# Optimization experiments

Measured on AMD Instinct MI355X. Metric: run time of the kernel, lower is better.

## Reference

```python
import jax, jax.numpy as jnp
import numpy as np

KERNEL_MUL = 2.0
KERNEL_NUM = 5


def setup_inputs() -> dict:
    key = jax.random.key(0)
    k1, k2 = jax.random.split(key)
    N, D = 4096, 256
    source = jax.random.normal(k1, (N, D), dtype=jnp.float32)
    target = jax.random.normal(k2, (N, D), dtype=jnp.float32)
    return {"source": source, "target": target}


def reference(source, target):
    ns = source.shape[0]
    total = jnp.concatenate([source, target], axis=0)  # [2N, D]
    n = total.shape[0]
    # Pairwise squared L2 distance via GEMM trick (same math as expand+sub+square+sum)
    sq = jnp.sum(total * total, axis=1)               # [2N]
    gram = total @ total.T                             # [2N, 2N]
    l2 = sq[:, None] + sq[None, :] - 2.0 * gram        # [2N, 2N]
    # Bandwidth from detached distances (torch uses .data)
    l2_sg = jax.lax.stop_gradient(l2)
    bandwidth = jnp.sum(l2_sg) / (n * n - n)
    bandwidth = bandwidth / (KERNEL_MUL ** (KERNEL_NUM // 2))
    bws = bandwidth * (KERNEL_MUL ** jnp.arange(KERNEL_NUM, dtype=l2.dtype))  # [K]
    # Multi-kernel Gaussian RBF sum: sum_k exp(-l2 / bw_k)
    kernels = jnp.exp(-l2[None, :, :] / bws[:, None, None]).sum(axis=0)  # [2N, 2N]
    XX = kernels[:ns, :ns]
    YY = kernels[ns:, ns:]
    XY = kernels[:ns, ns:]
    YX = kernels[ns:, :ns]
    loss = jnp.mean(XX) + jnp.mean(YY) - jnp.mean(XY) - jnp.mean(YX)
    return loss
```

## Files before the change

### kernel.cpp

```cpp
#include <hip/hip_runtime.h>
#include <hip/hip_bf16.h>
#include <stdint.h>


#define NROW 8192
#define NS   4096
#define DD   256
#define TILE 256
#define BK   64
#define NTB  32
#define NBLK (NTB*(NTB+1)/2)
#define K1B  128

typedef __bf16 bf16_t;
typedef __bf16 bf16x8 __attribute__((ext_vector_type(8)));
typedef __bf16 bf16x4 __attribute__((ext_vector_type(4)));
typedef float  f32x4  __attribute__((ext_vector_type(4)));
typedef float  f32x2  __attribute__((ext_vector_type(2)));

#define OFF_CPAR 0
#define OFF_SQ   1024
#define OFF_CS   (OFF_SQ + 8192*4)
#define OFF_SS   (OFF_CS + K1B*256*4)
#define OFF_TBF  (1<<18)

__device__ __forceinline__ void async16(const void* g, void* l) {
  __builtin_amdgcn_global_load_lds(
      (const __attribute__((address_space(1))) void*)(uintptr_t)g,
      (__attribute__((address_space(3))) void*)(uintptr_t)l, 16, 0, 0);
}

__global__ __launch_bounds__(256) void k1_prep(const float* __restrict__ src,
                                               const float* __restrict__ tgt,
                                               float* __restrict__ sq,
                                               float* __restrict__ cs_part,
                                               float* __restrict__ ss_part,
                                               bf16_t* __restrict__ tbf,
                                               float* __restrict__ out) {
  const int b = blockIdx.x, tid = threadIdx.x;
  const int w = tid >> 6, lane = tid & 63;
  if (b == 0 && tid == 0) out[0] = 0.f;
  float4 csum = make_float4(0.f, 0.f, 0.f, 0.f);
  float wss = 0.f;
  for (int r = 0; r < 16; ++r) {
    const int row = b * 64 + w * 16 + r;
    const float* rp = (row < NS) ? (src + (size_t)row * DD)
                                 : (tgt + (size_t)(row - NS) * DD);
    float4 v = ((const float4*)rp)[lane];
    bf16x4 o;
    o[0] = (bf16_t)v.x; o[1] = (bf16_t)v.y; o[2] = (bf16_t)v.z; o[3] = (bf16_t)v.w;
    *(bf16x4*)(tbf + (size_t)row * DD + lane * 4) = o;
    float s2 = v.x*v.x + v.y*v.y + v.z*v.z + v.w*v.w;
    #pragma unroll
    for (int off = 32; off >= 1; off >>= 1) s2 += __shfl_xor(s2, off);
    if (lane == 0) { sq[row] = s2; wss += s2; }
    csum.x += v.x; csum.y += v.y; csum.z += v.z; csum.w += v.w;
  }
  __shared__ float cls[4][256];
  __shared__ float sls[4];
  ((float4*)cls[w])[lane] = csum;
  if (lane == 0) sls[w] = wss;
  __syncthreads();
  cs_part[b * 256 + tid] = cls[0][tid] + cls[1][tid] + cls[2][tid] + cls[3][tid];
  if (tid == 0) ss_part[b] = sls[0] + sls[1] + sls[2] + sls[3];
}

__global__ __launch_bounds__(256) void k2_bw(const float* __restrict__ cs_part,
                                             const float* __restrict__ ss_part,
                                             float* __restrict__ cpar) {
  const int tid = threadIdx.x, w = tid >> 6, lane = tid & 63;
  float c = 0.f;
  for (int b = 0; b < K1B; ++b) c += cs_part[b * 256 + tid];
  double csq = (double)c * (double)c;
  double ssq = (tid < K1B) ? (double)ss_part[tid] : 0.0;
  #pragma unroll
  for (int off = 32; off >= 1; off >>= 1) {
    csq += __shfl_xor(csq, off);
    ssq += __shfl_xor(ssq, off);
  }
  __shared__ double rc[4], rs[4];
  if (lane == 0) { rc[w] = csq; rs[w] = ssq; }
  __syncthreads();
  if (tid == 0) {
    double C = rc[0] + rc[1] + rc[2] + rc[3];
    double S = rs[0] + rs[1] + rs[2] + rs[3];
    const double n = (double)NROW;
    double suml2 = 2.0 * n * S - 2.0 * C;
    double bw0 = suml2 / (n * n - n) / 4.0;
    cpar[0] = (float)(1.4426950408889634 / (16.0 * bw0));
  }
}

__global__ __launch_bounds__(512) void k3_mmd(const bf16_t* __restrict__ tbf,
                                              const float* __restrict__ sqg,
                                              const float* __restrict__ cpar,
                                              float* __restrict__ out) {
  __shared__ __align__(16) bf16_t As[TILE * BK];
  __shared__ __align__(16) bf16_t Bs[TILE * BK];
  __shared__ float red[8];

  const int t = blockIdx.x;
  int bi = (int)((sqrtf(8.0f * (float)t + 1.0f) - 1.0f) * 0.5f);
  while ((bi + 1) * (bi + 2) / 2 <= t) ++bi;
  while (bi * (bi + 1) / 2 > t) --bi;
  const int bj = t - bi * (bi + 1) / 2;

  const int tid = threadIdx.x;
  const int w = tid >> 6, lane = tid & 63;
  const int m0 = (w >> 2) * 128;
  const int n0 = (w & 3) * 64;
  const int wbase = tid & ~63;

  const float cE = cpar[0];

  f32x4 acc[8][4] = {};

  const bf16_t* Ag = tbf + (size_t)bi * TILE * DD;
  const bf16_t* Bg = tbf + (size_t)bj * TILE * DD;

  for (int kt = 0; kt < 4; ++kt) {
    __syncthreads();
    #pragma unroll
    for (int it = 0; it < 4; ++it) {
      const int c   = it * 512 + tid;
      const int r   = c >> 3;
      const int kcs = (c & 7) ^ (r & 7);
      async16(Ag + (size_t)r * DD + kt * 64 + kcs * 8,
              (char*)As + (size_t)(it * 512 + wbase) * 16);
      async16(Bg + (size_t)r * DD + kt * 64 + kcs * 8,
              (char*)Bs + (size_t)(it * 512 + wbase) * 16);
    }
    __syncthreads();
    #pragma unroll
    for (int kk = 0; kk < 2; ++kk) {
      const int kc = kk * 4 + (lane >> 4);
      const int kphys = (kc ^ (lane & 7)) * 8;
      bf16x8 af[8], bfr[4];
      #pragma unroll
      for (int mi = 0; mi < 8; ++mi)
        af[mi] = *(const bf16x8*)(As + (m0 + mi * 16 + (lane & 15)) * BK + kphys);
      #pragma unroll
      for (int ni = 0; ni < 4; ++ni)
        bfr[ni] = *(const bf16x8*)(Bs + (n0 + ni * 16 + (lane & 15)) * BK + kphys);
      #pragma unroll
      for (int mi = 0; mi < 8; ++mi)
        #pragma unroll
        for (int ni = 0; ni < 4; ++ni)
          acc[mi][ni] = __builtin_amdgcn_mfma_f32_16x16x32_bf16(
              af[mi], bfr[ni], acc[mi][ni], 0, 0, 0);
    }
  }

  const f32x2 c2 = {2.0f * cE, 2.0f * cE};
  f32x2 bj2[4];
  #pragma unroll
  for (int ni = 0; ni < 4; ++ni) {
    const float b = sqg[bj * TILE + n0 + ni * 16 + (lane & 15)] * cE;
    bj2[ni][0] = b; bj2[ni][1] = b;
  }

  f32x2 t2 = {0.f, 0.f};
  #pragma unroll
  for (int mi = 0; mi < 8; ++mi) {
    const int mbase = bi * TILE + m0 + mi * 16 + (lane >> 4) * 4;
    f32x2 ai2[2];
    ai2[0][0] = sqg[mbase + 0] * cE; ai2[0][1] = sqg[mbase + 1] * cE;
    ai2[1][0] = sqg[mbase + 2] * cE; ai2[1][1] = sqg[mbase + 3] * cE;
    #pragma unroll
    for (int ni = 0; ni < 4; ++ni) {
      #pragma unroll
      for (int h = 0; h < 2; ++h) {
        f32x2 g; g[0] = acc[mi][ni][2*h]; g[1] = acc[mi][ni][2*h+1];
        f32x2 e = g * c2 - (ai2[h] + bj2[ni]);
        f32x2 v;
        v[0] = __builtin_amdgcn_exp2f(e[0]);
        v[1] = __builtin_amdgcn_exp2f(e[1]);
        f32x2 v2 = v * v, v4 = v2 * v2, v8 = v4 * v4, v16 = v8 * v8;
        t2 += ((v + v2) + (v4 + v8)) + v16;
      }
    }
  }
  float tsum = t2[0] + t2[1];
  #pragma unroll
  for (int off = 32; off >= 1; off >>= 1) tsum += __shfl_xor(tsum, off);
  if (lane == 0) red[w] = tsum;
  __syncthreads();
  if (tid == 0) {
    float s = 0.f;
    #pragma unroll
    for (int i = 0; i < 8; ++i) s += red[i];
    const float sign = ((bi < NS / TILE) == (bj < NS / TILE)) ? 1.f : -1.f;
    const float wt   = (bi == bj) ? 1.f : 2.f;
    atomicAdd(out, s * sign * wt * (1.0f / ((float)NS * (float)NS)));
  }
}

extern "C" void kernel_launch(void* const* d_in, const int* in_sizes, int n_in,
                              void* d_out, int out_size, void* d_ws, size_t ws_size,
                              hipStream_t stream) {
  const float* src = (const float*)d_in[0];
  const float* tgt = (const float*)d_in[1];
  char* ws = (char*)d_ws;
  float*  cpar = (float*)(ws + OFF_CPAR);
  float*  sq   = (float*)(ws + OFF_SQ);
  float*  csp  = (float*)(ws + OFF_CS);
  float*  ssp  = (float*)(ws + OFF_SS);
  bf16_t* tbf  = (bf16_t*)(ws + OFF_TBF);
  float*  out  = (float*)d_out;

  k1_prep<<<K1B, 256, 0, stream>>>(src, tgt, sq, csp, ssp, tbf, out);
  k2_bw  <<<1,   256, 0, stream>>>(csp, ssp, cpar);
  k3_mmd <<<NBLK,512, 0, stream>>>(tbf, sq, cpar, out);
}
```

Baseline: 110.4 us.

## Pre-swizzle bf16 operands into MFMA fragment layout and drop LDS staging

The prep kernel now writes the bf16 copy of the inputs in a blocked layout matching the 16x16x32 MFMA operand fragments, so each lane loads its fragment directly from global memory with one 16-byte load. The GEMM kernel drops the LDS tiles, async loads and barriers, and switches to 128x128 tiles with 256 threads, giving about four times as many triangular blocks. The aim is to remove LDS round-trips and synchronisation and to spread work over more blocks, at the cost of more redundant global/L2 traffic, since each fragment is re-read by several waves and blocks without sharing.

```diff
diff --git a/kernel.cpp b/kernel.cpp
--- a/kernel.cpp
+++ b/kernel.cpp
@@ -6,15 +6,12 @@
 #define NROW 8192
 #define NS   4096
 #define DD   256
-#define TILE 256
-#define BK   64
-#define NTB  32
+#define NTB  64
 #define NBLK (NTB*(NTB+1)/2)
 #define K1B  128
 
 typedef __bf16 bf16_t;
 typedef __bf16 bf16x8 __attribute__((ext_vector_type(8)));
-typedef __bf16 bf16x4 __attribute__((ext_vector_type(4)));
 typedef float  f32x4  __attribute__((ext_vector_type(4)));
 typedef float  f32x2  __attribute__((ext_vector_type(2)));
 
@@ -23,12 +20,6 @@
 #define OFF_CS   (OFF_SQ + 8192*4)
 #define OFF_SS   (OFF_CS + K1B*256*4)
 #define OFF_TBF  (1<<18)
-
-__device__ __forceinline__ void async16(const void* g, void* l) {
-  __builtin_amdgcn_global_load_lds(
-      (const __attribute__((address_space(1))) void*)(uintptr_t)g,
-      (__attribute__((address_space(3))) void*)(uintptr_t)l, 16, 0, 0);
-}
 
 __global__ __launch_bounds__(256) void k1_prep(const float* __restrict__ src,
                                                const float* __restrict__ tgt,
@@ -38,28 +29,65 @@
                                                bf16_t* __restrict__ tbf,
                                                float* __restrict__ out) {
   const int b = blockIdx.x, tid = threadIdx.x;
-  const int w = tid >> 6, lane = tid & 63;
+  const int w = tid >> 6, l = tid & 63;
   if (b == 0 && tid == 0) out[0] = 0.f;
-  float4 csum = make_float4(0.f, 0.f, 0.f, 0.f);
+  const int lr = l >> 4;
+  const int lc = l & 15;
+  const int p  = b * 4 + w;
+
+  float cacc[2][8];
+  #pragma unroll
+  for (int a = 0; a < 2; ++a)
+    #pragma unroll
+    for (int j = 0; j < 8; ++j) cacc[a][j] = 0.f;
   float wss = 0.f;
-  for (int r = 0; r < 16; ++r) {
-    const int row = b * 64 + w * 16 + r;
+
+  for (int i = 0; i < 4; ++i) {
+    const int row = p * 16 + i * 4 + lr;
     const float* rp = (row < NS) ? (src + (size_t)row * DD)
                                  : (tgt + (size_t)(row - NS) * DD);
-    float4 v = ((const float4*)rp)[lane];
-    bf16x4 o;
-    o[0] = (bf16_t)v.x; o[1] = (bf16_t)v.y; o[2] = (bf16_t)v.z; o[3] = (bf16_t)v.w;
-    *(bf16x4*)(tbf + (size_t)row * DD + lane * 4) = o;
-    float s2 = v.x*v.x + v.y*v.y + v.z*v.z + v.w*v.w;
-    #pragma unroll
-    for (int off = 32; off >= 1; off >>= 1) s2 += __shfl_xor(s2, off);
-    if (lane == 0) { sq[row] = s2; wss += s2; }
-    csum.x += v.x; csum.y += v.y; csum.z += v.z; csum.w += v.w;
-  }
+    float rowsq = 0.f;
+    #pragma unroll
+    for (int a = 0; a < 2; ++a) {
+      const int c = a * 16 + lc;
+      float4 v0 = *(const float4*)(rp + c * 8);
+      float4 v1 = *(const float4*)(rp + c * 8 + 4);
+      bf16x8 o;
+      o[0]=(bf16_t)v0.x; o[1]=(bf16_t)v0.y; o[2]=(bf16_t)v0.z; o[3]=(bf16_t)v0.w;
+      o[4]=(bf16_t)v1.x; o[5]=(bf16_t)v1.y; o[6]=(bf16_t)v1.z; o[7]=(bf16_t)v1.w;
+      *(bf16x8*)(tbf + (size_t)p * 4096 + (c * 16 + i * 4 + lr) * 8) = o;
+      cacc[a][0]+=v0.x; cacc[a][1]+=v0.y; cacc[a][2]+=v0.z; cacc[a][3]+=v0.w;
+      cacc[a][4]+=v1.x; cacc[a][5]+=v1.y; cacc[a][6]+=v1.z; cacc[a][7]+=v1.w;
+      float s2 = v0.x*v0.x+v0.y*v0.y+v0.z*v0.z+v0.w*v0.w
+               + v1.x*v1.x+v1.y*v1.y+v1.z*v1.z+v1.w*v1.w;
+      #pragma unroll
+      for (int off = 1; off <= 8; off <<= 1) s2 += __shfl_xor(s2, off);
+      rowsq += s2;
+    }
+    if (lc == 0) { sq[row] = rowsq; wss += rowsq; }
+  }
+
+  #pragma unroll
+  for (int a = 0; a < 2; ++a)
+    #pragma unroll
+    for (int j = 0; j < 8; ++j) {
+      float v = cacc[a][j];
+      v += __shfl_xor(v, 16);
+      v += __shfl_xor(v, 32);
+      cacc[a][j] = v;
+    }
   __shared__ float cls[4][256];
   __shared__ float sls[4];
-  ((float4*)cls[w])[lane] = csum;
-  if (lane == 0) sls[w] = wss;
+  if (lr == 0) {
+    #pragma unroll
+    for (int a = 0; a < 2; ++a)
+      #pragma unroll
+      for (int j = 0; j < 8; ++j)
+        cls[w][(a * 16 + lc) * 8 + j] = cacc[a][j];
+  }
+  wss += __shfl_xor(wss, 16);
+  wss += __shfl_xor(wss, 32);
+  if (l == 0) sls[w] = wss;
   __syncthreads();
   cs_part[b * 256 + tid] = cls[0][tid] + cls[1][tid] + cls[2][tid] + cls[3][tid];
   if (tid == 0) ss_part[b] = sls[0] + sls[1] + sls[2] + sls[3];
@@ -91,13 +119,11 @@
   }
 }
 
-__global__ __launch_bounds__(512) void k3_mmd(const bf16_t* __restrict__ tbf,
+__global__ __launch_bounds__(256) void k3_mmd(const bf16_t* __restrict__ tbf,
                                               const float* __restrict__ sqg,
                                               const float* __restrict__ cpar,
                                               float* __restrict__ out) {
-  __shared__ __align__(16) bf16_t As[TILE * BK];
-  __shared__ __align__(16) bf16_t Bs[TILE * BK];
-  __shared__ float red[8];
+  __shared__ float red[4];
 
   const int t = blockIdx.x;
   int bi = (int)((sqrtf(8.0f * (float)t + 1.0f) - 1.0f) * 0.5f);
@@ -106,63 +132,46 @@
   const int bj = t - bi * (bi + 1) / 2;
 
   const int tid = threadIdx.x;
-  const int w = tid >> 6, lane = tid & 63;
-  const int m0 = (w >> 2) * 128;
-  const int n0 = (w & 3) * 64;
-  const int wbase = tid & ~63;
+  const int w = tid >> 6, l = tid & 63;
+  const int mh = w >> 1, nh = w & 1;
+  const int m0 = mh * 64, n0 = nh * 64;
 
   const float cE = cpar[0];
 
-  f32x4 acc[8][4] = {};
-
-  const bf16_t* Ag = tbf + (size_t)bi * TILE * DD;
-  const bf16_t* Bg = tbf + (size_t)bj * TILE * DD;
-
-  for (int kt = 0; kt < 4; ++kt) {
-    __syncthreads();
-    #pragma unroll
-    for (int it = 0; it < 4; ++it) {
-      const int c   = it * 512 + tid;
-      const int r   = c >> 3;
-      const int kcs = (c & 7) ^ (r & 7);
-      async16(Ag + (size_t)r * DD + kt * 64 + kcs * 8,
-              (char*)As + (size_t)(it * 512 + wbase) * 16);
-      async16(Bg + (size_t)r * DD + kt * 64 + kcs * 8,
-              (char*)Bs + (size_t)(it * 512 + wbase) * 16);
-    }
-    __syncthreads();
-    #pragma unroll
-    for (int kk = 0; kk < 2; ++kk) {
-      const int kc = kk * 4 + (lane >> 4);
-      const int kphys = (kc ^ (lane & 7)) * 8;
-      bf16x8 af[8], bfr[4];
-      #pragma unroll
-      for (int mi = 0; mi < 8; ++mi)
-        af[mi] = *(const bf16x8*)(As + (m0 + mi * 16 + (lane & 15)) * BK + kphys);
+  f32x4 acc[4][4] = {};
+
+  const bf16_t* Abase = tbf + (size_t)(bi * 8 + mh * 4) * 4096 + l * 8;
+  const bf16_t* Bbase = tbf + (size_t)(bj * 8 + nh * 4) * 4096 + l * 8;
+
+  #pragma unroll 2
+  for (int kk = 0; kk < 8; ++kk) {
+    bf16x8 af[4], bfr[4];
+    #pragma unroll
+    for (int mi = 0; mi < 4; ++mi)
+      af[mi] = *(const bf16x8*)(Abase + mi * 4096 + kk * 512);
+    #pragma unroll
+    for (int ni = 0; ni < 4; ++ni)
+      bfr[ni] = *(const bf16x8*)(Bbase + ni * 4096 + kk * 512);
+    #pragma unroll
+    for (int mi = 0; mi < 4; ++mi)
       #pragma unroll
       for (int ni = 0; ni < 4; ++ni)
-        bfr[ni] = *(const bf16x8*)(Bs + (n0 + ni * 16 + (lane & 15)) * BK + kphys);
-      #pragma unroll
-      for (int mi = 0; mi < 8; ++mi)
-        #pragma unroll
-        for (int ni = 0; ni < 4; ++ni)
-          acc[mi][ni] = __builtin_amdgcn_mfma_f32_16x16x32_bf16(
-              af[mi], bfr[ni], acc[mi][ni], 0, 0, 0);
-    }
+        acc[mi][ni] = __builtin_amdgcn_mfma_f32_16x16x32_bf16(
+            af[mi], bfr[ni], acc[mi][ni], 0, 0, 0);
   }
 
   const f32x2 c2 = {2.0f * cE, 2.0f * cE};
   f32x2 bj2[4];
   #pragma unroll
   for (int ni = 0; ni < 4; ++ni) {
-    const float b = sqg[bj * TILE + n0 + ni * 16 + (lane & 15)] * cE;
+    const float b = sqg[bj * 128 + n0 + ni * 16 + (l & 15)] * cE;
     bj2[ni][0] = b; bj2[ni][1] = b;
   }
 
   f32x2 t2 = {0.f, 0.f};
   #pragma unroll
-  for (int mi = 0; mi < 8; ++mi) {
-    const int mbase = bi * TILE + m0 + mi * 16 + (lane >> 4) * 4;
+  for (int mi = 0; mi < 4; ++mi) {
+    const int mbase = bi * 128 + m0 + mi * 16 + (l >> 4) * 4;
     f32x2 ai2[2];
     ai2[0][0] = sqg[mbase + 0] * cE; ai2[0][1] = sqg[mbase + 1] * cE;
     ai2[1][0] = sqg[mbase + 2] * cE; ai2[1][1] = sqg[mbase + 3] * cE;
@@ -183,13 +192,11 @@
   float tsum = t2[0] + t2[1];
   #pragma unroll
   for (int off = 32; off >= 1; off >>= 1) tsum += __shfl_xor(tsum, off);
-  if (lane == 0) red[w] = tsum;
+  if (l == 0) red[w] = tsum;
   __syncthreads();
   if (tid == 0) {
-    float s = 0.f;
-    #pragma unroll
-    for (int i = 0; i < 8; ++i) s += red[i];
-    const float sign = ((bi < NS / TILE) == (bj < NS / TILE)) ? 1.f : -1.f;
+    const float s    = red[0] + red[1] + red[2] + red[3];
+    const float sign = ((bi < NS / 128) == (bj < NS / 128)) ? 1.f : -1.f;
     const float wt   = (bi == bj) ? 1.f : 2.f;
     atomicAdd(out, s * sign * wt * (1.0f / ((float)NS * (float)NS)));
   }
@@ -210,5 +217,5 @@
 
   k1_prep<<<K1B, 256, 0, stream>>>(src, tgt, sq, csp, ssp, tbf, out);
   k2_bw  <<<1,   256, 0, stream>>>(csp, ssp, cpar);
-  k3_mmd <<<NBLK,512, 0, stream>>>(tbf, sq, cpar, out);
-}
+  k3_mmd <<<NBLK,256, 0, stream>>>(tbf, sq, cpar, out);
+}
```

Result: no change. 110.7 us (+0.3%).
